# Optimization experiments

Measured on AMD Instinct MI355X. Metric: run time of the kernel, lower is better.

## Reference

```python
import jax, jax.numpy as jnp
import numpy as np
from jax import lax

BETA = 1.0
UNITS = 1024
FT_DIM = 512
TIME = 256
BATCH = 128


def setup_inputs() -> dict:
    key = jax.random.key(0)
    k1, k2, k3 = jax.random.split(key, 3)
    inputs = jax.random.normal(k1, (BATCH, TIME, FT_DIM), dtype=jnp.float32)
    # R ~ RandomNormal(stddev=1/time_horizon)
    R = jax.random.normal(k2, (FT_DIM, UNITS), dtype=jnp.float32) * (1.0 / TIME)
    # W ~ Orthogonal initializer
    A = jax.random.normal(k3, (UNITS, UNITS), dtype=jnp.float32)
    W, _ = jnp.linalg.qr(A)
    bias = jnp.zeros((UNITS,), dtype=jnp.float32)
    x0 = jnp.zeros((UNITS,), dtype=jnp.float32)
    return {"inputs": inputs, "R": R, "W": W, "bias": bias, "x0": x0}


def reference(inputs, R, W, bias, x0):
    B = inputs.shape[0]
    # Precompute input projections for all steps: [B, T, U]
    h_in = jnp.einsum('btf,fu->btu', inputs, R) + bias

    def step(state, h_t):  # state: [B,U], h_t: [B,U]
        s = jnp.tanh(h_t + state @ W)
        return s, s

    state0 = jnp.broadcast_to(x0, (B, x0.shape[0]))
    _, states_t = lax.scan(step, state0, jnp.swapaxes(h_in, 0, 1))  # [T,B,U]
    states = jnp.swapaxes(states_t, 0, 1)  # [B,T,U]

    # Tilted smoothing: per example, (1/beta)*log(tanh(mean_t exp(beta*s_t)))
    terminal = (1.0 / BETA) * jnp.log(jnp.tanh(jnp.mean(jnp.exp(BETA * states), axis=1)))  # [B,U]

    # Original returns list of T per-step states plus terminal; return stacked [B, T+1, U]
    return jnp.concatenate([states, terminal[:, None, :]], axis=1)
```

## Files before the change

kernel.cpp:

```cpp
#include <hip/hip_runtime.h>
#include <hip/hip_bf16.h>

#define B_ 128
#define T_ 256
#define F_ 512
#define U_ 1024

typedef __attribute__((ext_vector_type(8))) short short8;
typedef __attribute__((ext_vector_type(4))) float f32x4;
typedef unsigned long long u64;


#define SB_REGION 16384

__global__ __launch_bounds__(256) void init_kernel(
    const float* __restrict__ x0, short* __restrict__ shi,
    short* __restrict__ slo, int* __restrict__ wsbar) {
  const int tid = threadIdx.x;
  if (blockIdx.x == 0) { wsbar[tid] = 0; wsbar[tid + 256] = 0; }
  const int idx = blockIdx.x * 256 + tid;
  const int k   = idx & 1023;
  const int row = (idx >> 10) & 15;
  const int g   = idx >> 14;
  const float x = x0[k];
  const unsigned ux = __float_as_uint(x);
  const unsigned h  = ux & 0xFFFF0000u;
  const float l     = x - __uint_as_float(h);
  const size_t sidx = (size_t)(g * 2 + 1) * SB_REGION + ((size_t)(k >> 3) * 16 + row) * 8 + (k & 7);
  shi[sidx] = (short)(h >> 16);
  slo[sidx] = (short)(__float_as_uint(l) >> 16);
}

__global__ __launch_bounds__(256) void winit_kernel(
    const float* __restrict__ W, short* __restrict__ wsWh,
    short* __restrict__ wsWl) {
  const int idx = blockIdx.x * 256 + threadIdx.x;
  const int u = idx & 1023;
  const int k = idx >> 10;
  const float x = W[(size_t)k * U_ + u];
  const unsigned ux = __float_as_uint(x);
  const unsigned h  = ux & 0xFFFF0000u;
  const float l     = x - __uint_as_float(h);
  const int cb = u >> 6, nt = (u >> 4) & 3;
  const int kh = k >> 9, ks = (k >> 5) & 15;
  const int ln = (((k >> 3) & 3) << 4) | (u & 15);
  const size_t w = ((size_t)((((cb * 4 + nt) * 2 + kh) * 16 + ks)) * 64 + ln) * 8 + (k & 7);
  wsWh[w] = (short)(h >> 16);
  wsWl[w] = (short)(__float_as_uint(l) >> 16);
}

__global__ __launch_bounds__(256) void hproj_kernel(
    const float* __restrict__ inp, const float* __restrict__ R,
    const float* __restrict__ bias, float* __restrict__ out) {
  __shared__ short bt_hi[64][40];
  __shared__ short bt_lo[64][40];

  const int tid  = threadIdx.x;
  const int mblk = blockIdx.x >> 4;
  const int nblk = blockIdx.x & 15;
  const int n0   = nblk * 64;
  const int wave = tid >> 6, lane = tid & 63;
  const int lm   = lane & 15, quad = lane >> 4;
  const int r0   = mblk * 64 + wave * 16;

  f32x4 c[4] = {{0,0,0,0},{0,0,0,0},{0,0,0,0},{0,0,0,0}};

  for (int kc = 0; kc < 16; ++kc) {
    const int k0 = kc * 32;
    {
      const int kr = tid >> 3;
      const int ns = (tid & 7) * 8;
      const float* p = R + (size_t)(k0 + kr) * U_ + n0 + ns;
      float4 va = *(const float4*)p;
      float4 vb = *(const float4*)(p + 4);
      float v[8] = {va.x, va.y, va.z, va.w, vb.x, vb.y, vb.z, vb.w};
#pragma unroll
      for (int i = 0; i < 8; ++i) {
        const unsigned ux = __float_as_uint(v[i]);
        const unsigned h  = ux & 0xFFFF0000u;
        const float l     = v[i] - __uint_as_float(h);
        bt_hi[ns + i][kr] = (short)(h >> 16);
        bt_lo[ns + i][kr] = (short)(__float_as_uint(l) >> 16);
      }
    }
    __syncthreads();

    const float* ap = inp + (size_t)(r0 + lm) * F_ + k0 + quad * 8;
    float4 aa = *(const float4*)ap;
    float4 ab = *(const float4*)(ap + 4);
    float av[8] = {aa.x, aa.y, aa.z, aa.w, ab.x, ab.y, ab.z, ab.w};
    short8 ahi, alo;
#pragma unroll
    for (int i = 0; i < 8; ++i) {
      const unsigned ux = __float_as_uint(av[i]);
      const unsigned h  = ux & 0xFFFF0000u;
      const float l     = av[i] - __uint_as_float(h);
      ahi[i] = (short)(h >> 16);
      alo[i] = (short)(__float_as_uint(l) >> 16);
    }

#pragma unroll
    for (int nt = 0; nt < 4; ++nt) {
      short8 bhi = *(const short8*)&bt_hi[nt * 16 + lm][quad * 8];
      short8 blo = *(const short8*)&bt_lo[nt * 16 + lm][quad * 8];
      c[nt] = __builtin_amdgcn_mfma_f32_16x16x32_bf16(ahi, bhi, c[nt], 0, 0, 0);
      c[nt] = __builtin_amdgcn_mfma_f32_16x16x32_bf16(ahi, blo, c[nt], 0, 0, 0);
      c[nt] = __builtin_amdgcn_mfma_f32_16x16x32_bf16(alo, bhi, c[nt], 0, 0, 0);
    }
    __syncthreads();
  }

#pragma unroll
  for (int nt = 0; nt < 4; ++nt) {
    const int u = n0 + nt * 16 + lm;
    const float bv = bias[u];
#pragma unroll
    for (int r = 0; r < 4; ++r) {
      const int row = r0 + quad * 4 + r;
      const int b   = row >> 8;
      out[(size_t)(row + b) * U_ + u] = c[nt][r] + bv;
    }
  }
}

__global__ __launch_bounds__(512, 2) void recur_kernel(
    const short* __restrict__ wsWh, const short* __restrict__ wsWl,
    float* __restrict__ out, int* __restrict__ wsbar,
    short* __restrict__ shi, short* __restrict__ slo) {
  __shared__ short lds_h[SB_REGION];
  __shared__ short lds_l[SB_REGION];
  __shared__ float red[4 * 64 * 4];
  __shared__ float sstage[16 * 64];

  const int tid  = threadIdx.x;
  const int wv   = tid >> 6, lane = tid & 63;
  const int lm   = lane & 15, quad = lane >> 4;
  const int nt   = wv & 3, kh = wv >> 2;
  const int g    = blockIdx.x & 7;
  const int cb   = blockIdx.x >> 3;
  const int u    = cb * 64 + nt * 16 + lm;

  short8 wh[16], wl[16];
  {
    const size_t wbase = ((size_t)(((cb * 4 + nt) * 2 + kh) * 16) * 64 + lane) * 8;
#pragma unroll
    for (int ks = 0; ks < 16; ++ks) {
      wh[ks] = *(const short8*)(wsWh + wbase + (size_t)ks * 512);
      wl[ks] = *(const short8*)(wsWl + wbase + (size_t)ks * 512);
    }
  }

  float accE[4] = {0.f, 0.f, 0.f, 0.f};
  int* const cntp = wsbar + 256 + g * 32;
  const size_t gbase = (size_t)g * 2 * SB_REGION;

  const int pt     = tid & 255;
  const int cs_row = (pt * 4) >> 6;
  const int cs_ug  = cb * 64 + ((pt * 4) & 63);
  const size_t cs_dst = ((size_t)(cs_ug >> 3) * 16 + cs_row) * 8 + (cs_ug & 7);

  for (int t = 0; t < T_; ++t) {
    const int pr = (t + 1) & 1;
    const int pw = t & 1;

    float hv[4] = {0.f, 0.f, 0.f, 0.f};
    if (kh == 0) {
#pragma unroll
      for (int r = 0; r < 4; ++r) {
        const int row = g * 16 + quad * 4 + r;
        hv[r] = out[((size_t)row * 257 + t) * U_ + u];
      }
    }

    {
      const u64* gh = (const u64*)(shi + gbase + (size_t)pr * SB_REGION);
      const u64* gl = (const u64*)(slo + gbase + (size_t)pr * SB_REGION);
      u64 rh[8], rl[8];
#pragma unroll
      for (int i = 0; i < 8; ++i)
        rh[i] = __hip_atomic_load(gh + i * 512 + tid, __ATOMIC_RELAXED,
                                  __HIP_MEMORY_SCOPE_AGENT);
#pragma unroll
      for (int i = 0; i < 8; ++i)
        rl[i] = __hip_atomic_load(gl + i * 512 + tid, __ATOMIC_RELAXED,
                                  __HIP_MEMORY_SCOPE_AGENT);
      u64* lh = (u64*)lds_h;
      u64* ll = (u64*)lds_l;
#pragma unroll
      for (int i = 0; i < 8; ++i) lh[i * 512 + tid] = rh[i];
#pragma unroll
      for (int i = 0; i < 8; ++i) ll[i * 512 + tid] = rl[i];
    }
    __syncthreads();

    f32x4 c = {0, 0, 0, 0};
#pragma unroll
    for (int ks = 0; ks < 16; ++ks) {
      const int off = (((kh * 16 + ks) * 4 + quad) * 16 + lm) * 8;
      short8 ah = *(const short8*)&lds_h[off];
      short8 al = *(const short8*)&lds_l[off];
      c = __builtin_amdgcn_mfma_f32_16x16x32_bf16(ah, wh[ks], c, 0, 0, 0);
      c = __builtin_amdgcn_mfma_f32_16x16x32_bf16(ah, wl[ks], c, 0, 0, 0);
      c = __builtin_amdgcn_mfma_f32_16x16x32_bf16(al, wh[ks], c, 0, 0, 0);
    }
    if (kh == 1) *(f32x4*)&red[(nt * 64 + lane) * 4] = c;
    __syncthreads();

    if (kh == 0) {
      f32x4 p = *(const f32x4*)&red[(nt * 64 + lane) * 4];
      c += p;
#pragma unroll
      for (int r = 0; r < 4; ++r) {
        const int row15 = quad * 4 + r;
        const int row   = g * 16 + row15;
        const float s   = tanhf(c[r] + hv[r]);
        out[((size_t)row * 257 + t) * U_ + u] = s;
        accE[r] += __expf(s);
        sstage[row15 * 64 + (nt * 16 + lm)] = s;
      }
    }
    __syncthreads();

    if (kh == 1) {
      float4 sv = *(const float4*)&sstage[pt * 4];
      float v[4] = {sv.x, sv.y, sv.z, sv.w};
      u64 ph = 0, pl = 0;
#pragma unroll
      for (int j = 0; j < 4; ++j) {
        const unsigned ux = __float_as_uint(v[j]);
        const unsigned h  = ux & 0xFFFF0000u;
        const float l     = v[j] - __uint_as_float(h);
        ph |= (u64)(unsigned short)(h >> 16) << (16 * j);
        pl |= (u64)(unsigned short)(__float_as_uint(l) >> 16) << (16 * j);
      }
      u64* dsth = (u64*)(shi + gbase + (size_t)pw * SB_REGION + cs_dst);
      u64* dstl = (u64*)(slo + gbase + (size_t)pw * SB_REGION + cs_dst);
      __hip_atomic_store(dsth, ph, __ATOMIC_RELAXED, __HIP_MEMORY_SCOPE_AGENT);
      __hip_atomic_store(dstl, pl, __ATOMIC_RELAXED, __HIP_MEMORY_SCOPE_AGENT);
    }
    asm volatile("s_waitcnt vmcnt(0)" ::: "memory");
    __syncthreads();

    if (tid == 0) {
      const int prev = __hip_atomic_fetch_add(cntp, 1, __ATOMIC_RELAXED,
                                              __HIP_MEMORY_SCOPE_AGENT);
      const int target = 16 * (t + 1);
      if (prev != target - 1) {
        while (__hip_atomic_load(cntp, __ATOMIC_RELAXED,
                                 __HIP_MEMORY_SCOPE_AGENT) < target) {
          __builtin_amdgcn_s_sleep(1);
        }
      }
    }
    __syncthreads();
  }

  if (kh == 0) {
#pragma unroll
    for (int r = 0; r < 4; ++r) {
      const int row = g * 16 + quad * 4 + r;
      out[((size_t)row * 257 + T_) * U_ + u] = logf(tanhf(accE[r] * (1.0f / 256.0f)));
    }
  }
}

extern "C" void kernel_launch(void* const* d_in, const int* in_sizes, int n_in,
                              void* d_out, int out_size, void* d_ws, size_t ws_size,
                              hipStream_t stream) {
  (void)in_sizes; (void)n_in; (void)out_size; (void)ws_size;
  const float* inp  = (const float*)d_in[0];
  const float* R    = (const float*)d_in[1];
  const float* W    = (const float*)d_in[2];
  const float* bias = (const float*)d_in[3];
  const float* x0   = (const float*)d_in[4];
  float* out = (float*)d_out;
  int*   wsbar = (int*)d_ws;
  short* shi  = (short*)((char*)d_ws + 2048);
  short* slo  = shi + 8 * 2 * SB_REGION;
  short* wsWh = slo + 8 * 2 * SB_REGION;
  short* wsWl = wsWh + 1024 * 1024;

  init_kernel<<<dim3(512), dim3(256), 0, stream>>>(x0, shi, slo, wsbar);
  winit_kernel<<<dim3(4096), dim3(256), 0, stream>>>(W, wsWh, wsWl);
  hproj_kernel<<<dim3(8192), dim3(256), 0, stream>>>(inp, R, bias, out);
  recur_kernel<<<dim3(128), dim3(512), 0, stream>>>(wsWh, wsWl, out, wsbar, shi, slo);
}
```

Measured before the change: 1.396 ms.

## Retile input projection with 32x32 MFMA and streamline recurrent grid barrier

The input projection now converts R once into a pre-split bf16 hi/lo MFMA layout in a separate kernel. The projection itself uses 128x256 tiles built on 32x32x16 MFMA, which cuts redundant conversion work and raises reuse. In the recurrent kernel, each wave signals arrival through an LDS counter and only the last one bumps the global counter. Every wave then spins on that counter itself, so the block-wide syncthreads around the barrier and the final step's publish are dropped. The next step's h_in is prefetched during the wait, and three independent accumulators break the MFMA dependency chain. This adds workspace and one extra launch, and relies on per-wave spinning with relaxed atomics for correctness.

New measurement: 1.667 ms. +19.4%, slower.

```diff
diff --git a/kernel.cpp b/kernel.cpp
--- a/kernel.cpp
+++ b/kernel.cpp
@@ -8,6 +8,7 @@
 
 typedef __attribute__((ext_vector_type(8))) short short8;
 typedef __attribute__((ext_vector_type(4))) float f32x4;
+typedef __attribute__((ext_vector_type(16))) float f32x16;
 typedef unsigned long long u64;
 
 
@@ -49,76 +50,95 @@
   wsWl[w] = (short)(__float_as_uint(l) >> 16);
 }
 
+__global__ __launch_bounds__(256) void rinit_kernel(
+    const float* __restrict__ R, short* __restrict__ rsh,
+    short* __restrict__ rsl) {
+  const int idx = blockIdx.x * 256 + threadIdx.x;
+  const int u = idx & 1023;
+  const int k = idx >> 10;
+  const float x = R[(size_t)k * U_ + u];
+  const unsigned ux = __float_as_uint(x);
+  const unsigned h  = ux & 0xFFFF0000u;
+  const float l     = x - __uint_as_float(h);
+  const int ub = u >> 5;
+  const int kt = k >> 4;
+  const int ln = (((k >> 3) & 1) << 5) | (u & 31);
+  const size_t w = ((size_t)(ub * 32 + kt) * 64 + ln) * 8 + (k & 7);
+  rsh[w] = (short)(h >> 16);
+  rsl[w] = (short)(__float_as_uint(l) >> 16);
+}
+
 __global__ __launch_bounds__(256) void hproj_kernel(
-    const float* __restrict__ inp, const float* __restrict__ R,
-    const float* __restrict__ bias, float* __restrict__ out) {
-  __shared__ short bt_hi[64][40];
-  __shared__ short bt_lo[64][40];
+    const float* __restrict__ inp, const short* __restrict__ rsh,
+    const short* __restrict__ rsl, const float* __restrict__ bias,
+    float* __restrict__ out) {
+  __shared__ __align__(16) short bs[32 * 512];
 
   const int tid  = threadIdx.x;
-  const int mblk = blockIdx.x >> 4;
-  const int nblk = blockIdx.x & 15;
-  const int n0   = nblk * 64;
-  const int wave = tid >> 6, lane = tid & 63;
-  const int lm   = lane & 15, quad = lane >> 4;
-  const int r0   = mblk * 64 + wave * 16;
-
-  f32x4 c[4] = {{0,0,0,0},{0,0,0,0},{0,0,0,0},{0,0,0,0}};
+  const int wv   = tid >> 6, lane = tid & 63;
+  const int mblk = blockIdx.x >> 2;
+  const int nblk = blockIdx.x & 3;
+  const int row0 = mblk * 128 + wv * 32;
+  const int arow = row0 + (lane & 31);
+  const int asub = (lane >> 5) * 8;
+
+  f32x16 c[8] = {};
 
   for (int kc = 0; kc < 16; ++kc) {
-    const int k0 = kc * 32;
-    {
-      const int kr = tid >> 3;
-      const int ns = (tid & 7) * 8;
-      const float* p = R + (size_t)(k0 + kr) * U_ + n0 + ns;
-      float4 va = *(const float4*)p;
-      float4 vb = *(const float4*)(p + 4);
-      float v[8] = {va.x, va.y, va.z, va.w, vb.x, vb.y, vb.z, vb.w};
-#pragma unroll
-      for (int i = 0; i < 8; ++i) {
-        const unsigned ux = __float_as_uint(v[i]);
+    __syncthreads();
+#pragma unroll
+    for (int i = 0; i < 8; ++i) {
+      const int cidx = i * 4 + wv;
+      const int a    = cidx >> 4;
+      const int ntc  = (cidx >> 1) & 7;
+      const int ktl  = cidx & 1;
+      const short* src = (a ? rsl : rsh) +
+          ((size_t)((nblk * 8 + ntc) * 32 + kc * 2 + ktl) * 64 + lane) * 8;
+      *(short8*)&bs[cidx * 512 + lane * 8] = *(const short8*)src;
+    }
+    __syncthreads();
+
+    short8 ah[2], al[2];
+#pragma unroll
+    for (int kt = 0; kt < 2; ++kt) {
+      const float* ap = inp + (size_t)arow * F_ + kc * 32 + kt * 16 + asub;
+      float4 a0 = *(const float4*)ap;
+      float4 a1 = *(const float4*)(ap + 4);
+      float av[8] = {a0.x, a0.y, a0.z, a0.w, a1.x, a1.y, a1.z, a1.w};
+#pragma unroll
+      for (int j = 0; j < 8; ++j) {
+        const unsigned ux = __float_as_uint(av[j]);
         const unsigned h  = ux & 0xFFFF0000u;
-        const float l     = v[i] - __uint_as_float(h);
-        bt_hi[ns + i][kr] = (short)(h >> 16);
-        bt_lo[ns + i][kr] = (short)(__float_as_uint(l) >> 16);
-      }
-    }
-    __syncthreads();
-
-    const float* ap = inp + (size_t)(r0 + lm) * F_ + k0 + quad * 8;
-    float4 aa = *(const float4*)ap;
-    float4 ab = *(const float4*)(ap + 4);
-    float av[8] = {aa.x, aa.y, aa.z, aa.w, ab.x, ab.y, ab.z, ab.w};
-    short8 ahi, alo;
-#pragma unroll
-    for (int i = 0; i < 8; ++i) {
-      const unsigned ux = __float_as_uint(av[i]);
-      const unsigned h  = ux & 0xFFFF0000u;
-      const float l     = av[i] - __uint_as_float(h);
-      ahi[i] = (short)(h >> 16);
-      alo[i] = (short)(__float_as_uint(l) >> 16);
-    }
-
-#pragma unroll
-    for (int nt = 0; nt < 4; ++nt) {
-      short8 bhi = *(const short8*)&bt_hi[nt * 16 + lm][quad * 8];
-      short8 blo = *(const short8*)&bt_lo[nt * 16 + lm][quad * 8];
-      c[nt] = __builtin_amdgcn_mfma_f32_16x16x32_bf16(ahi, bhi, c[nt], 0, 0, 0);
-      c[nt] = __builtin_amdgcn_mfma_f32_16x16x32_bf16(ahi, blo, c[nt], 0, 0, 0);
-      c[nt] = __builtin_amdgcn_mfma_f32_16x16x32_bf16(alo, bhi, c[nt], 0, 0, 0);
-    }
-    __syncthreads();
-  }
-
-#pragma unroll
-  for (int nt = 0; nt < 4; ++nt) {
-    const int u = n0 + nt * 16 + lm;
+        const float l     = av[j] - __uint_as_float(h);
+        ah[kt][j] = (short)(h >> 16);
+        al[kt][j] = (short)(__float_as_uint(l) >> 16);
+      }
+    }
+
+#pragma unroll
+    for (int ntt = 0; ntt < 8; ++ntt) {
+#pragma unroll
+      for (int kt = 0; kt < 2; ++kt) {
+        short8 bh = *(const short8*)&bs[((0 * 8 + ntt) * 2 + kt) * 512 + lane * 8];
+        short8 bl = *(const short8*)&bs[((1 * 8 + ntt) * 2 + kt) * 512 + lane * 8];
+        c[ntt] = __builtin_amdgcn_mfma_f32_32x32x16_bf16(ah[kt], bh, c[ntt], 0, 0, 0);
+        c[ntt] = __builtin_amdgcn_mfma_f32_32x32x16_bf16(ah[kt], bl, c[ntt], 0, 0, 0);
+        c[ntt] = __builtin_amdgcn_mfma_f32_32x32x16_bf16(al[kt], bh, c[ntt], 0, 0, 0);
+      }
+    }
+  }
+
+  const int crow0 = row0 + 4 * (lane >> 5);
+  const int cu    = nblk * 256 + (lane & 31);
+#pragma unroll
+  for (int ntt = 0; ntt < 8; ++ntt) {
+    const int u = cu + ntt * 32;
     const float bv = bias[u];
 #pragma unroll
-    for (int r = 0; r < 4; ++r) {
-      const int row = r0 + quad * 4 + r;
+    for (int reg = 0; reg < 16; ++reg) {
+      const int row = crow0 + (reg & 3) + 8 * (reg >> 2);
       const int b   = row >> 8;
-      out[(size_t)(row + b) * U_ + u] = c[nt][r] + bv;
+      out[(size_t)(row + b) * U_ + u] = c[ntt][reg] + bv;
     }
   }
 }
@@ -131,6 +151,7 @@
   __shared__ short lds_l[SB_REGION];
   __shared__ float red[4 * 64 * 4];
   __shared__ float sstage[16 * 64];
+  __shared__ int   lcnt;
 
   const int tid  = threadIdx.x;
   const int wv   = tid >> 6, lane = tid & 63;
@@ -140,6 +161,8 @@
   const int cb   = blockIdx.x >> 3;
   const int u    = cb * 64 + nt * 16 + lm;
 
+  if (tid == 0) lcnt = 0;
+
   short8 wh[16], wl[16];
   {
     const size_t wbase = ((size_t)(((cb * 4 + nt) * 2 + kh) * 16) * 64 + lane) * 8;
@@ -159,18 +182,18 @@
   const int cs_ug  = cb * 64 + ((pt * 4) & 63);
   const size_t cs_dst = ((size_t)(cs_ug >> 3) * 16 + cs_row) * 8 + (cs_ug & 7);
 
+  float hv[4] = {0.f, 0.f, 0.f, 0.f};
+  if (kh == 0) {
+#pragma unroll
+    for (int r = 0; r < 4; ++r) {
+      const int row = g * 16 + quad * 4 + r;
+      hv[r] = out[((size_t)row * 257 + 0) * U_ + u];
+    }
+  }
+
   for (int t = 0; t < T_; ++t) {
     const int pr = (t + 1) & 1;
     const int pw = t & 1;
-
-    float hv[4] = {0.f, 0.f, 0.f, 0.f};
-    if (kh == 0) {
-#pragma unroll
-      for (int r = 0; r < 4; ++r) {
-        const int row = g * 16 + quad * 4 + r;
-        hv[r] = out[((size_t)row * 257 + t) * U_ + u];
-      }
-    }
 
     {
       const u64* gh = (const u64*)(shi + gbase + (size_t)pr * SB_REGION);
@@ -193,16 +216,17 @@
     }
     __syncthreads();
 
-    f32x4 c = {0, 0, 0, 0};
+    f32x4 c0 = {0, 0, 0, 0}, c1 = {0, 0, 0, 0}, c2 = {0, 0, 0, 0};
 #pragma unroll
     for (int ks = 0; ks < 16; ++ks) {
       const int off = (((kh * 16 + ks) * 4 + quad) * 16 + lm) * 8;
       short8 ah = *(const short8*)&lds_h[off];
       short8 al = *(const short8*)&lds_l[off];
-      c = __builtin_amdgcn_mfma_f32_16x16x32_bf16(ah, wh[ks], c, 0, 0, 0);
-      c = __builtin_amdgcn_mfma_f32_16x16x32_bf16(ah, wl[ks], c, 0, 0, 0);
-      c = __builtin_amdgcn_mfma_f32_16x16x32_bf16(al, wh[ks], c, 0, 0, 0);
-    }
+      c0 = __builtin_amdgcn_mfma_f32_16x16x32_bf16(ah, wh[ks], c0, 0, 0, 0);
+      c1 = __builtin_amdgcn_mfma_f32_16x16x32_bf16(ah, wl[ks], c1, 0, 0, 0);
+      c2 = __builtin_amdgcn_mfma_f32_16x16x32_bf16(al, wh[ks], c2, 0, 0, 0);
+    }
+    f32x4 c = (c0 + c1) + c2;
     if (kh == 1) *(f32x4*)&red[(nt * 64 + lane) * 4] = c;
     __syncthreads();
 
@@ -221,38 +245,48 @@
     }
     __syncthreads();
 
-    if (kh == 1) {
-      float4 sv = *(const float4*)&sstage[pt * 4];
-      float v[4] = {sv.x, sv.y, sv.z, sv.w};
-      u64 ph = 0, pl = 0;
-#pragma unroll
-      for (int j = 0; j < 4; ++j) {
-        const unsigned ux = __float_as_uint(v[j]);
-        const unsigned h  = ux & 0xFFFF0000u;
-        const float l     = v[j] - __uint_as_float(h);
-        ph |= (u64)(unsigned short)(h >> 16) << (16 * j);
-        pl |= (u64)(unsigned short)(__float_as_uint(l) >> 16) << (16 * j);
-      }
-      u64* dsth = (u64*)(shi + gbase + (size_t)pw * SB_REGION + cs_dst);
-      u64* dstl = (u64*)(slo + gbase + (size_t)pw * SB_REGION + cs_dst);
-      __hip_atomic_store(dsth, ph, __ATOMIC_RELAXED, __HIP_MEMORY_SCOPE_AGENT);
-      __hip_atomic_store(dstl, pl, __ATOMIC_RELAXED, __HIP_MEMORY_SCOPE_AGENT);
-    }
-    asm volatile("s_waitcnt vmcnt(0)" ::: "memory");
-    __syncthreads();
-
-    if (tid == 0) {
-      const int prev = __hip_atomic_fetch_add(cntp, 1, __ATOMIC_RELAXED,
-                                              __HIP_MEMORY_SCOPE_AGENT);
+    if (t != T_ - 1) {
+      if (kh == 1) {
+        float4 sv = *(const float4*)&sstage[pt * 4];
+        float v[4] = {sv.x, sv.y, sv.z, sv.w};
+        u64 ph = 0, pl = 0;
+#pragma unroll
+        for (int j = 0; j < 4; ++j) {
+          const unsigned ux = __float_as_uint(v[j]);
+          const unsigned h  = ux & 0xFFFF0000u;
+          const float l     = v[j] - __uint_as_float(h);
+          ph |= (u64)(unsigned short)(h >> 16) << (16 * j);
+          pl |= (u64)(unsigned short)(__float_as_uint(l) >> 16) << (16 * j);
+        }
+        u64* dsth = (u64*)(shi + gbase + (size_t)pw * SB_REGION + cs_dst);
+        u64* dstl = (u64*)(slo + gbase + (size_t)pw * SB_REGION + cs_dst);
+        __hip_atomic_store(dsth, ph, __ATOMIC_RELAXED, __HIP_MEMORY_SCOPE_AGENT);
+        __hip_atomic_store(dstl, pl, __ATOMIC_RELAXED, __HIP_MEMORY_SCOPE_AGENT);
+        asm volatile("s_waitcnt vmcnt(0)" ::: "memory");
+        if (lane == 0) {
+          const int prev = atomicAdd(&lcnt, 1);
+          if (prev == 4 * t + 3)
+            __hip_atomic_fetch_add(cntp, 1, __ATOMIC_RELAXED,
+                                   __HIP_MEMORY_SCOPE_AGENT);
+        }
+      } else {
+#pragma unroll
+        for (int r = 0; r < 4; ++r) {
+          const int row = g * 16 + quad * 4 + r;
+          hv[r] = out[((size_t)row * 257 + (t + 1)) * U_ + u];
+        }
+      }
+
       const int target = 16 * (t + 1);
-      if (prev != target - 1) {
-        while (__hip_atomic_load(cntp, __ATOMIC_RELAXED,
-                                 __HIP_MEMORY_SCOPE_AGENT) < target) {
-          __builtin_amdgcn_s_sleep(1);
-        }
-      }
-    }
-    __syncthreads();
+      int vcnt = __hip_atomic_load(cntp, __ATOMIC_RELAXED,
+                                   __HIP_MEMORY_SCOPE_AGENT);
+      while (vcnt < target) {
+        __builtin_amdgcn_s_sleep(1);
+        vcnt = __hip_atomic_load(cntp, __ATOMIC_RELAXED,
+                                 __HIP_MEMORY_SCOPE_AGENT);
+      }
+      asm volatile("" ::: "memory");
+    }
   }
 
   if (kh == 0) {
@@ -279,9 +313,12 @@
   short* slo  = shi + 8 * 2 * SB_REGION;
   short* wsWh = slo + 8 * 2 * SB_REGION;
   short* wsWl = wsWh + 1024 * 1024;
+  short* rsh  = wsWl + 1024 * 1024;
+  short* rsl  = rsh + 512 * 1024;
 
   init_kernel<<<dim3(512), dim3(256), 0, stream>>>(x0, shi, slo, wsbar);
   winit_kernel<<<dim3(4096), dim3(256), 0, stream>>>(W, wsWh, wsWl);
-  hproj_kernel<<<dim3(8192), dim3(256), 0, stream>>>(inp, R, bias, out);
+  rinit_kernel<<<dim3(2048), dim3(256), 0, stream>>>(R, rsh, rsl);
+  hproj_kernel<<<dim3(1024), dim3(256), 0, stream>>>(inp, rsh, rsl, bias, out);
   recur_kernel<<<dim3(128), dim3(512), 0, stream>>>(wsWh, wsWl, out, wsbar, shi, slo);
 }
```
